# Optimization experiments

Measured on AMD Instinct MI355X. Metric: run time of the kernel, lower is better.

Reference implementation:

```python
import math
import jax, jax.numpy as jnp
import numpy as np

X_DIM = 512
Y_DIM = 512
DS = 4
WH, WW = Y_DIM // DS, X_DIM // DS
RADIUS = 6          # search_radius
PATCH = 21          # patch_size
SIGMA = 1.0         # preprocess_sigma
DELTA = 0.2
MASK_TH = 0.05
RAIN_TH = 0.1


def _blur(x, sigma=SIGMA):
    # replicate-pad + depthwise 2D gaussian conv (matches _gaussian_blur2d)
    r = max(1, int(math.ceil(3.0 * sigma)))
    c = jnp.arange(-r, r + 1, dtype=x.dtype)
    k1 = jnp.exp(-(c * c) / (2.0 * sigma * sigma))
    k1 = k1 / jnp.sum(k1)
    k2 = jnp.outer(k1, k1)
    C = x.shape[1]
    kern = jnp.broadcast_to(k2[None, None], (C, 1, 2 * r + 1, 2 * r + 1))
    xp = jnp.pad(x, ((0, 0), (0, 0), (r, r), (r, r)), mode='edge')
    return jax.lax.conv_general_dilated(xp, kern, (1, 1), 'VALID',
                                        dimension_numbers=('NCHW', 'OIHW', 'NCHW'),
                                        feature_group_count=C)


def _resize(x, oh, ow):
    # torch bilinear, align_corners=False, no antialias
    ih, iw = x.shape[-2], x.shape[-1]
    def coords(o, i):
        s = (jnp.arange(o, dtype=jnp.float32) + 0.5) * (i / o) - 0.5
        s = jnp.maximum(s, 0.0)
        i0 = jnp.minimum(jnp.floor(s).astype(jnp.int32), i - 1)
        i1 = jnp.minimum(i0 + 1, i - 1)
        return i0, i1, s - i0.astype(jnp.float32)
    y0, y1, wy = coords(oh, ih)
    x0, x1, wx = coords(ow, iw)
    r0 = x[..., y0, :]
    r1 = x[..., y1, :]
    v00 = r0[..., x0]; v01 = r0[..., x1]
    v10 = r1[..., x0]; v11 = r1[..., x1]
    wy = wy[:, None]; wx = wx[None, :]
    return v00 * (1 - wy) * (1 - wx) + v01 * (1 - wy) * wx + v10 * wy * (1 - wx) + v11 * wy * wx


def _avg_pool(x, k):
    # avg_pool2d, stride 1, padding k//2, count_include_pad=True
    p = k // 2
    nd = x.ndim
    win = (1,) * (nd - 2) + (k, k)
    pads = ((0, 0),) * (nd - 2) + ((p, p), (p, p))
    s = jax.lax.reduce_window(x, 0.0, jax.lax.add, win, (1,) * nd, pads)
    return s / float(k * k)


def _prepare(f):
    w = jnp.log1p(jnp.maximum(f, 0.0))
    w = _resize(w, WH, WW)
    return _blur(w)


def _grid_sample_border(field, grid):
    # bilinear grid_sample, padding_mode='border', align_corners=True
    B, C, H, W = field.shape
    ix = jnp.clip((grid[..., 0] + 1.0) * 0.5 * (W - 1), 0.0, W - 1)
    iy = jnp.clip((grid[..., 1] + 1.0) * 0.5 * (H - 1), 0.0, H - 1)
    x0 = jnp.floor(ix).astype(jnp.int32); y0 = jnp.floor(iy).astype(jnp.int32)
    x1 = jnp.minimum(x0 + 1, W - 1); y1 = jnp.minimum(y0 + 1, H - 1)
    wx = (ix - x0)[..., None]; wy = (iy - y0)[..., None]
    b = jnp.arange(B)[:, None, None]
    v00 = field[b, :, y0, x0]; v01 = field[b, :, y0, x1]
    v10 = field[b, :, y1, x0]; v11 = field[b, :, y1, x1]  # each [B,H,W,C]
    out = v00 * (1 - wy) * (1 - wx) + v01 * (1 - wy) * wx + v10 * wy * (1 - wx) + v11 * wy * wx
    return jnp.transpose(out, (0, 3, 1, 2))


def setup_inputs() -> dict:
    key = jax.random.key(0)
    k1, k2, k3 = jax.random.split(key, 3)
    pred = jax.random.normal(k1, (16, 1, 512, 512), dtype=jnp.float32)
    target = jax.random.uniform(k2, (16, 1, 512, 512), dtype=jnp.float32)
    ref = jax.random.uniform(k3, (16, 1, 512, 512), dtype=jnp.float32)
    return {"pred": pred, "target": target, "ref": ref}


def reference(pred, target, ref):
    prev_w = _prepare(ref)      # [B,1,WH,WW]
    curr_w = _prepare(target)
    rain = (_resize(target, WH, WW) >= RAIN_TH).astype(jnp.float32)
    n = 2 * RADIUS + 1
    offs = jnp.arange(-RADIUS, RADIUS + 1)
    dys = jnp.repeat(offs, n)   # dy outer loop
    dxs = jnp.tile(offs, n)     # dx inner loop
    rows = jnp.arange(WH); cols = jnp.arange(WW)

    def shift_cost(dy, dx):
        # replicate-border shift of curr_w by (dy,dx), then local SSD (21x21 avg)
        sh = curr_w[:, :, jnp.clip(rows + dy, 0, WH - 1), :]
        sh = sh[:, :, :, jnp.clip(cols + dx, 0, WW - 1)]
        return _avg_pool((prev_w - sh) ** 2, PATCH)

    costs = jax.vmap(shift_cost)(dys, dxs)        # [S,B,1,WH,WW]
    best = jnp.argmin(costs, axis=0)[:, 0]        # [B,WH,WW] (first-min, matches torch)
    fx = dxs.astype(jnp.float32)[best][:, None] * rain   # [B,1,WH,WW]
    fy = dys.astype(jnp.float32)[best][:, None] * rain
    fx = _blur(fx) * rain
    fy = _blur(fy) * rain
    fx = _resize(fx, Y_DIM, X_DIM) * (X_DIM / WW)
    fy = _resize(fy, Y_DIM, X_DIM) * (Y_DIM / WH)

    yy, xx = jnp.meshgrid(jnp.linspace(-1.0, 1.0, Y_DIM),
                          jnp.linspace(-1.0, 1.0, X_DIM), indexing='ij')
    gx = xx[None] - fx[:, 0] * (2.0 / (X_DIM - 1))
    gy = yy[None] - fy[:, 0] * (2.0 / (Y_DIM - 1))
    teacher = jnp.maximum(_grid_sample_border(ref, jnp.stack([gx, gy], axis=-1)), 0.0)

    d = pred - teacher
    ad = jnp.abs(d)
    loss = jnp.where(ad < DELTA, 0.5 * d * d, DELTA * (ad - 0.5 * DELTA))  # huber
    mask = ((teacher > MASK_TH) | (target > MASK_TH)).astype(loss.dtype)
    return jnp.mean(loss * mask)
```

## Files before the change

kernel.cpp:

```cpp
#include <hip/hip_runtime.h>
#include <math.h>

#define BATCH 16
#define HR 512
#define LR 128
#define N_LR (BATCH*LR*LR)
#define N_HR (BATCH*HR*HR)
#define NSH 13
#define NSHIFT 169
#define TH 8
#define CW 16

__device__ __forceinline__ int clampi(int v, int lo, int hi){ return v<lo?lo:(v>hi?hi:v); }

__device__ __forceinline__ float gk(int t){
  const float e1 = 0.60653065971263342f;
  const float e2 = 0.13533528323661270f;
  const float e3 = 0.011108996538242306f;
  const float norm = 1.0f/(1.0f + 2.0f*(e1+e2+e3));
  int a = t < 0 ? -t : t;
  float v = (a==0) ? 1.0f : (a==1 ? e1 : (a==2 ? e2 : e3));
  return v*norm;
}

__global__ void k_downsample(const float* __restrict__ ref, const float* __restrict__ tar,
                             float* __restrict__ wref, float* __restrict__ wtar,
                             float* __restrict__ rain){
  int i = blockIdx.x*blockDim.x + threadIdx.x;
  if (i >= N_LR) return;
  int x = i & (LR-1); int y = (i >> 7) & (LR-1); int b = i >> 14;
  int base = b*HR*HR + (4*y+1)*HR + 4*x;
  float4 r1 = *(const float4*)(ref + base);
  float4 r2 = *(const float4*)(ref + base + HR);
  float4 t1 = *(const float4*)(tar + base);
  float4 t2 = *(const float4*)(tar + base + HR);
  float r00=r1.y, r01=r1.z, r10=r2.y, r11=r2.z;
  float t00=t1.y, t01=t1.z, t10=t2.y, t11=t2.z;
  wref[i] = 0.25f*(log1pf(fmaxf(r00,0.f))+log1pf(fmaxf(r01,0.f))
                 +log1pf(fmaxf(r10,0.f))+log1pf(fmaxf(r11,0.f)));
  wtar[i] = 0.25f*(log1pf(fmaxf(t00,0.f))+log1pf(fmaxf(t01,0.f))
                 +log1pf(fmaxf(t10,0.f))+log1pf(fmaxf(t11,0.f)));
  rain[i] = (0.25f*(t00+t01+t10+t11) >= 0.1f) ? 1.0f : 0.0f;
}

__global__ void k_blur2(const float* __restrict__ in0, const float* __restrict__ in1,
                        float* __restrict__ out0, float* __restrict__ out1,
                        const float* __restrict__ m0, const float* __restrict__ m1){
  const int z = blockIdx.z;
  const float* in  = z ? in1 : in0;
  float* out       = z ? out1 : out0;
  const float* msk = z ? m1 : m0;
  const int r0 = blockIdx.x * 16;
  const int bb = blockIdx.y;
  const int tid = threadIdx.x;
  const float* I = in + (bb<<14);
  __shared__ float raw[22][LR];
  __shared__ float hb[22][LR];
  for (int idx = tid; idx < 22*LR; idx += 256){
    int lr = idx >> 7, c = idx & (LR-1);
    int gr = clampi(r0 - 3 + lr, 0, LR-1);
    raw[lr][c] = I[(gr<<7) + c];
  }
  __syncthreads();
  for (int idx = tid; idx < 22*LR; idx += 256){
    int lr = idx >> 7, c = idx & (LR-1);
    float s = 0.f;
    #pragma unroll
    for (int t=-3;t<=3;++t) s += gk(t)*raw[lr][clampi(c+t,0,LR-1)];
    hb[lr][c] = s;
  }
  __syncthreads();
  for (int idx = tid; idx < 16*LR; idx += 256){
    int lr = idx >> 7, c = idx & (LR-1);
    int i = r0 + lr;
    float s = 0.f;
    #pragma unroll
    for (int t=-3;t<=3;++t) s += gk(t)*hb[clampi(i+t,0,LR-1) - (r0-3)][c];
    int gi = (bb<<14) + (i<<7) + c;
    if (msk) s *= msk[gi];
    out[gi] = s;
  }
}

__global__ void __launch_bounds__(1024)
k_cost_flow(const float* __restrict__ prev, const float* __restrict__ curr,
            const float* __restrict__ rain,
            float* __restrict__ fx, float* __restrict__ fy){
  const int r0 = blockIdx.x * TH;
  const int bb = blockIdx.y;
  const int tid = threadIdx.x;
  const int w = tid >> 6, lane = tid & 63;
  const int j0 = 2*lane;
  const float* P = prev + (bb<<14);
  const float* C = curr + (bb<<14);

  __shared__ __align__(16) union {
    struct { float prevT[28][LR]; float currT[40][140]; } t;
    unsigned long long merge[4][TH*LR];
  } sh;
  __shared__ float pfx[CW][LR];

  for (int idx = tid; idx < 28*LR; idx += 1024){
    int lr = idx >> 7, c = idx & (LR-1);
    int gr = r0 - 10 + lr;
    if (gr >= 0 && gr < LR) sh.t.prevT[lr][c] = P[(gr<<7) + c];
  }
  for (int idx = tid; idx < 40*140; idx += 1024){
    int lr = idx / 140, c = idx - lr*140;
    int gr = r0 - 16 + lr;
    if (gr >= 0 && gr < LR) sh.t.currT[lr][c] = C[(gr<<7) + clampi(c-6,0,LR-1)];
  }
  __syncthreads();

  unsigned long long bk0[TH], bk1[TH];
  #pragma unroll
  for (int io=0; io<TH; ++io){ bk0[io] = ~0ULL; bk1[io] = ~0ULL; }

  for (int s = w; s < NSHIFT; s += CW){
    const int dy = s/NSH - 6, dx = s%NSH - 6;
    const int cb = dx + 6;
    float V0[TH], V1[TH];
    float v0 = 0.f, v1 = 0.f;
    #pragma unroll
    for (int u = -10; u <= 10; ++u){
      int r = r0 + u;
      if (r < 0 || r >= LR) continue;
      int lr = u + 10;
      int cr = clampi(r + dy, 0, LR-1) - r0 + 16;
      float2 p = *(const float2*)&sh.t.prevT[lr][j0];
      float c0 = sh.t.currT[cr][j0 + cb];
      float c1 = sh.t.currT[cr][j0 + 1 + cb];
      float d0 = p.x - c0, d1 = p.y - c1;
      v0 = fmaf(d0,d0,v0); v1 = fmaf(d1,d1,v1);
    }
    V0[0] = v0; V1[0] = v1;
    #pragma unroll
    for (int io = 1; io < TH; ++io){
      int i = r0 + io;
      int ra = i + 10;
      if (ra < LR){
        int lr = ra - r0 + 10;
        int cr = clampi(ra + dy, 0, LR-1) - r0 + 16;
        float2 p = *(const float2*)&sh.t.prevT[lr][j0];
        float c0 = sh.t.currT[cr][j0 + cb];
        float c1 = sh.t.currT[cr][j0 + 1 + cb];
        float d0 = p.x - c0, d1 = p.y - c1;
        v0 = fmaf(d0,d0,v0); v1 = fmaf(d1,d1,v1);
      }
      int rs = i - 11;
      if (rs >= 0){
        int lr = rs - r0 + 10;
        int cr = clampi(rs + dy, 0, LR-1) - r0 + 16;
        float2 p = *(const float2*)&sh.t.prevT[lr][j0];
        float c0 = sh.t.currT[cr][j0 + cb];
        float c1 = sh.t.currT[cr][j0 + 1 + cb];
        float d0 = p.x - c0, d1 = p.y - c1;
        v0 -= d0*d0; v1 -= d1*d1;
      }
      V0[io] = v0; V1[io] = v1;
    }
    #pragma unroll
    for (int io = 0; io < TH; ++io){
      float t = V0[io] + V1[io];
      float x = t;
      #pragma unroll
      for (int d = 1; d < 64; d <<= 1){
        float y = __shfl_up(x, d, 64);
        if (lane >= d) x += y;
      }
      float excl = x - t;
      float p0 = excl + V0[io];
      float p1 = p0 + V1[io];
      *(float2*)&pfx[w][j0] = make_float2(p0, p1);
      float a0 = pfx[w][min(j0+10, LR-1)];
      float a1 = pfx[w][min(j0+11, LR-1)];
      float b0r = pfx[w][max(j0-11, 0)];
      float b1r = pfx[w][max(j0-10, 0)];
      float b0 = (j0 >= 11) ? b0r : 0.f;
      float b1 = (j0 >= 10) ? b1r : 0.f;
      float c0 = fmaxf((a0-b0)*(1.0f/441.0f), 0.f);
      float c1 = fmaxf((a1-b1)*(1.0f/441.0f), 0.f);
      unsigned long long k0 = ((unsigned long long)__float_as_uint(c0)<<32) | (unsigned)s;
      unsigned long long k1 = ((unsigned long long)__float_as_uint(c1)<<32) | (unsigned)s;
      if (k0 < bk0[io]) bk0[io] = k0;
      if (k1 < bk1[io]) bk1[io] = k1;
    }
  }

  __syncthreads();
  const int g = w & 3;
  #pragma unroll
  for (int round = 0; round < 4; ++round){
    if ((w >> 2) == round){
      if (round == 0){
        #pragma unroll
        for (int io = 0; io < TH; ++io){
          sh.merge[g][io*LR + j0]     = bk0[io];
          sh.merge[g][io*LR + j0 + 1] = bk1[io];
        }
      } else {
        #pragma unroll
        for (int io = 0; io < TH; ++io){
          unsigned long long m0 = sh.merge[g][io*LR + j0];
          unsigned long long m1 = sh.merge[g][io*LR + j0 + 1];
          sh.merge[g][io*LR + j0]     = (bk0[io] < m0) ? bk0[io] : m0;
          sh.merge[g][io*LR + j0 + 1] = (bk1[io] < m1) ? bk1[io] : m1;
        }
      }
    }
    __syncthreads();
  }
  {
    int p = tid;
    unsigned long long k = sh.merge[0][p];
    unsigned long long k1 = sh.merge[1][p]; if (k1 < k) k = k1;
    unsigned long long k2 = sh.merge[2][p]; if (k2 < k) k = k2;
    unsigned long long k3 = sh.merge[3][p]; if (k3 < k) k = k3;
    int s = (int)(k & 0xffffffffULL);
    int io = p >> 7, jj = p & (LR-1);
    int gi = (bb<<14) + ((r0+io)<<7) + jj;
    float r = rain[gi];
    fx[gi] = (float)(s % NSH - 6) * r;
    fy[gi] = (float)(s / NSH - 6) * r;
  }
}

__global__ void __launch_bounds__(256)
k_loss(const float* __restrict__ pred, const float* __restrict__ tar,
       const float* __restrict__ ref, const float* __restrict__ fxb,
       const float* __restrict__ fyb, float* __restrict__ out){
  const int nthreads = gridDim.x * 256;
  float acc = 0.f;
  for (int gq = blockIdx.x*256 + threadIdx.x; gq < N_HR/4; gq += nthreads){
    int b   = gq >> 16;
    int rem = gq & 65535;
    int y   = rem >> 7;
    int x4  = (rem & 127) << 2;
    float sy = fmaxf(0.25f*(float)y - 0.375f, 0.f);
    int y0 = min((int)sy, LR-1); int y1 = min(y0+1, LR-1); float wy = sy - (float)y0;
    int lb = b<<14;
    const float* Fx0 = fxb + lb + (y0<<7);
    const float* Fx1 = fxb + lb + (y1<<7);
    const float* Fy0 = fyb + lb + (y0<<7);
    const float* Fy1 = fyb + lb + (y1<<7);
    int hb = (b<<18) + (y<<9) + x4;
    float4 pd = *(const float4*)(pred + hb);
    float4 td = *(const float4*)(tar + hb);
    const float* R = ref + (b<<18);
    #pragma unroll
    for (int k = 0; k < 4; ++k){
      int x = x4 + k;
      float sx = fmaxf(0.25f*(float)x - 0.375f, 0.f);
      int x0 = min((int)sx, LR-1); int x1 = min(x0+1, LR-1); float wx = sx - (float)x0;
      float w00=(1.f-wy)*(1.f-wx), w01=(1.f-wy)*wx, w10=wy*(1.f-wx), w11=wy*wx;
      float fxv = 4.f*(w00*Fx0[x0] + w01*Fx0[x1] + w10*Fx1[x0] + w11*Fx1[x1]);
      float fyv = 4.f*(w00*Fy0[x0] + w01*Fy0[x1] + w10*Fy1[x0] + w11*Fy1[x1]);
      float ix = fminf(fmaxf((float)x - fxv, 0.f), (float)(HR-1));
      float iy = fminf(fmaxf((float)y - fyv, 0.f), (float)(HR-1));
      int gx0 = (int)ix; int gx1 = min(gx0+1, HR-1); float gwx = ix - (float)gx0;
      int gy0 = (int)iy; int gy1 = min(gy0+1, HR-1); float gwy = iy - (float)gy0;
      float v00 = R[(gy0<<9)+gx0], v01 = R[(gy0<<9)+gx1];
      float v10 = R[(gy1<<9)+gx0], v11 = R[(gy1<<9)+gx1];
      float t = v00*(1.f-gwy)*(1.f-gwx) + v01*(1.f-gwy)*gwx
              + v10*gwy*(1.f-gwx)       + v11*gwy*gwx;
      float teacher = fmaxf(t, 0.f);
      float pk = ((const float*)&pd)[k];
      float tk = ((const float*)&td)[k];
      float d  = pk - teacher;
      float ad = fabsf(d);
      float l  = ad < 0.2f ? 0.5f*d*d : 0.2f*(ad - 0.1f);
      float m  = (teacher > 0.05f || tk > 0.05f) ? 1.f : 0.f;
      acc += l*m;
    }
  }
  acc *= (1.0f/(float)N_HR);
  #pragma unroll
  for (int o = 32; o > 0; o >>= 1) acc += __shfl_down(acc, o, 64);
  __shared__ float wsum[4];
  int lane = threadIdx.x & 63, wv = threadIdx.x >> 6;
  if (lane == 0) wsum[wv] = acc;
  __syncthreads();
  if (threadIdx.x == 0) atomicAdd(out, wsum[0]+wsum[1]+wsum[2]+wsum[3]);
}

extern "C" void kernel_launch(void* const* d_in, const int* in_sizes, int n_in,
                              void* d_out, int out_size, void* d_ws, size_t ws_size,
                              hipStream_t stream){
  const float* pred = (const float*)d_in[0];
  const float* tar  = (const float*)d_in[1];
  const float* ref  = (const float*)d_in[2];
  float* out = (float*)d_out;
  float* w = (float*)d_ws;
  float* prevW = w + 0*N_LR;
  float* currW = w + 1*N_LR;
  float* rain  = w + 2*N_LR;
  float* fxb   = w + 3*N_LR;
  float* fyb   = w + 4*N_LR;
  float* dsA   = w + 5*N_LR;
  float* dsB   = w + 6*N_LR;

  hipMemsetAsync(d_out, 0, sizeof(float), stream);

  const int tb = 256, nb = (N_LR + tb - 1)/tb;
  k_downsample<<<nb, tb, 0, stream>>>(ref, tar, dsA, dsB, rain);
  k_blur2<<<dim3(8, BATCH, 2), tb, 0, stream>>>(dsA, dsB, prevW, currW, nullptr, nullptr);
  k_cost_flow<<<dim3(LR/TH, BATCH), 1024, 0, stream>>>(prevW, currW, rain, dsA, dsB);
  k_blur2<<<dim3(8, BATCH, 2), tb, 0, stream>>>(dsA, dsB, fxb, fyb, rain, rain);
  k_loss<<<2048, tb, 0, stream>>>(pred, tar, ref, fxb, fyb, out);
}
```

Baseline: 217.2 us.

## Restructure cost-flow with register-resident rows, DPP prefix scans, and simplified loss upsampling

New measurement: 191.2 us. -11.9%, faster.

```diff
diff --git a/kernel.cpp b/kernel.cpp
--- a/kernel.cpp
+++ b/kernel.cpp
@@ -9,7 +9,7 @@
 #define NSH 13
 #define NSHIFT 169
 #define TH 8
-#define CW 16
+#define NW 8
 
 __device__ __forceinline__ int clampi(int v, int lo, int hi){ return v<lo?lo:(v>hi?hi:v); }
 
@@ -82,7 +82,45 @@
   }
 }
 
-__global__ void __launch_bounds__(1024)
+template<int CTRL, int RM>
+__device__ __forceinline__ float dpp_mov0(float x){
+  return __int_as_float(__builtin_amdgcn_update_dpp(0, __float_as_int(x), CTRL, RM, 0xF, true));
+}
+__device__ __forceinline__ float prefix64(float x){
+  x += dpp_mov0<0x111,0xF>(x);
+  x += dpp_mov0<0x112,0xF>(x);
+  x += dpp_mov0<0x114,0xF>(x);
+  x += dpp_mov0<0x118,0xF>(x);
+  x += dpp_mov0<0x142,0xA>(x);
+  x += dpp_mov0<0x143,0xC>(x);
+  return x;
+}
+__device__ __forceinline__ float bperm(int addr4, float v){
+  return __int_as_float(__builtin_amdgcn_ds_bpermute(addr4, __float_as_int(v)));
+}
+
+struct TapCtx { int ia0, ib0, ia1, ib1; bool la0hi, lb0ok, lb1hi, selA, selB; };
+
+__device__ __forceinline__ void horiz_update(const TapCtx& tc, float v0, float v1, int s,
+                                             unsigned long long& k0ref, unsigned long long& k1ref){
+  float pf0 = prefix64(v0);
+  float pf1 = prefix64(v1);
+  float T0 = __int_as_float(__builtin_amdgcn_readlane(__float_as_int(pf0), 63));
+  float va = tc.selA ? pf0 : pf1;
+  float vb = tc.selB ? pf0 : pf1;
+  float a0 = bperm(tc.ia0, va) + (tc.la0hi ? T0 : 0.f);
+  float b0 = tc.lb0ok ? bperm(tc.ib0, pf0) : 0.f;
+  float a1 = bperm(tc.ia1, pf1) + T0;
+  float b1 = bperm(tc.ib1, vb) + (tc.lb1hi ? T0 : 0.f);
+  float c0 = fmaxf((a0 - b0) * (1.0f/441.0f), 0.f);
+  float c1 = fmaxf((a1 - b1) * (1.0f/441.0f), 0.f);
+  unsigned long long k0 = ((unsigned long long)__float_as_uint(c0) << 32) | (unsigned)s;
+  unsigned long long k1 = ((unsigned long long)__float_as_uint(c1) << 32) | (unsigned)s;
+  if (k0 < k0ref) k0ref = k0;
+  if (k1 < k1ref) k1ref = k1;
+}
+
+__global__ void __launch_bounds__(512, 2)
 k_cost_flow(const float* __restrict__ prev, const float* __restrict__ curr,
             const float* __restrict__ rain,
             float* __restrict__ fx, float* __restrict__ fy){
@@ -90,132 +128,128 @@
   const int bb = blockIdx.y;
   const int tid = threadIdx.x;
   const int w = tid >> 6, lane = tid & 63;
-  const int j0 = 2*lane;
   const float* P = prev + (bb<<14);
   const float* C = curr + (bb<<14);
 
-  __shared__ __align__(16) union {
-    struct { float prevT[28][LR]; float currT[40][140]; } t;
-    unsigned long long merge[4][TH*LR];
-  } sh;
-  __shared__ float pfx[CW][LR];
-
-  for (int idx = tid; idx < 28*LR; idx += 1024){
+  __shared__ float currT[40][LR];
+  __shared__ unsigned long long mg[4][TH*LR];
+
+  for (int idx = tid; idx < 40*LR; idx += 512){
     int lr = idx >> 7, c = idx & (LR-1);
-    int gr = r0 - 10 + lr;
-    if (gr >= 0 && gr < LR) sh.t.prevT[lr][c] = P[(gr<<7) + c];
-  }
-  for (int idx = tid; idx < 40*140; idx += 1024){
-    int lr = idx / 140, c = idx - lr*140;
-    int gr = r0 - 16 + lr;
-    if (gr >= 0 && gr < LR) sh.t.currT[lr][c] = C[(gr<<7) + clampi(c-6,0,LR-1)];
+    int gr = clampi(r0 - 16 + lr, 0, LR-1);
+    currT[lr][c] = C[(gr<<7) + c];
+  }
+
+  float p0[28], p1[28];
+  #pragma unroll
+  for (int wr = 0; wr < 28; ++wr){
+    int gr = r0 - 10 + wr;
+    if (gr >= 0 && gr < LR){ p0[wr] = P[(gr<<7) + lane]; p1[wr] = P[(gr<<7) + lane + 64]; }
+    else                   { p0[wr] = 0.f; p1[wr] = 0.f; }
   }
   __syncthreads();
 
   unsigned long long bk0[TH], bk1[TH];
   #pragma unroll
-  for (int io=0; io<TH; ++io){ bk0[io] = ~0ULL; bk1[io] = ~0ULL; }
-
-  for (int s = w; s < NSHIFT; s += CW){
-    const int dy = s/NSH - 6, dx = s%NSH - 6;
-    const int cb = dx + 6;
-    float V0[TH], V1[TH];
-    float v0 = 0.f, v1 = 0.f;
-    #pragma unroll
-    for (int u = -10; u <= 10; ++u){
-      int r = r0 + u;
-      if (r < 0 || r >= LR) continue;
-      int lr = u + 10;
-      int cr = clampi(r + dy, 0, LR-1) - r0 + 16;
-      float2 p = *(const float2*)&sh.t.prevT[lr][j0];
-      float c0 = sh.t.currT[cr][j0 + cb];
-      float c1 = sh.t.currT[cr][j0 + 1 + cb];
-      float d0 = p.x - c0, d1 = p.y - c1;
-      v0 = fmaf(d0,d0,v0); v1 = fmaf(d1,d1,v1);
-    }
-    V0[0] = v0; V1[0] = v1;
-    #pragma unroll
-    for (int io = 1; io < TH; ++io){
-      int i = r0 + io;
-      int ra = i + 10;
-      if (ra < LR){
-        int lr = ra - r0 + 10;
-        int cr = clampi(ra + dy, 0, LR-1) - r0 + 16;
-        float2 p = *(const float2*)&sh.t.prevT[lr][j0];
-        float c0 = sh.t.currT[cr][j0 + cb];
-        float c1 = sh.t.currT[cr][j0 + 1 + cb];
-        float d0 = p.x - c0, d1 = p.y - c1;
-        v0 = fmaf(d0,d0,v0); v1 = fmaf(d1,d1,v1);
-      }
-      int rs = i - 11;
-      if (rs >= 0){
-        int lr = rs - r0 + 10;
-        int cr = clampi(rs + dy, 0, LR-1) - r0 + 16;
-        float2 p = *(const float2*)&sh.t.prevT[lr][j0];
-        float c0 = sh.t.currT[cr][j0 + cb];
-        float c1 = sh.t.currT[cr][j0 + 1 + cb];
-        float d0 = p.x - c0, d1 = p.y - c1;
-        v0 -= d0*d0; v1 -= d1*d1;
-      }
-      V0[io] = v0; V1[io] = v1;
-    }
-    #pragma unroll
-    for (int io = 0; io < TH; ++io){
-      float t = V0[io] + V1[io];
-      float x = t;
+  for (int io = 0; io < TH; ++io){ bk0[io] = ~0ULL; bk1[io] = ~0ULL; }
+
+  TapCtx tc;
+  tc.ia0 = ((lane + 10) & 63) << 2;
+  tc.ib0 = ((lane - 11) & 63) << 2;
+  tc.ia1 = (min(lane + 10, 63)) << 2;
+  tc.ib1 = ((lane + 53) & 63) << 2;
+  tc.la0hi = (lane >= 54);
+  tc.lb0ok = (lane >= 11);
+  tc.lb1hi = (lane >= 11);
+  tc.selA  = (lane >= 10);
+  tc.selB  = (lane >= 53);
+
+  const int t_lo = (NSHIFT * w) / NW;
+  const int t_hi = (NSHIFT * (w+1)) / NW;
+
+  int t = t_lo;
+  while (t < t_hi){
+    const int dxi  = t / NSH;
+    const int dyi0 = t - dxi*NSH;
+    const int ndy  = min(NSH - dyi0, t_hi - t);
+    const int dx   = dxi - 6;
+    const int c0   = clampi(lane + dx, 0, LR-1);
+    const int c1   = clampi(lane + 64 + dx, 0, LR-1);
+    float q0[28], q1[28];
+    #pragma unroll
+    for (int wr = 0; wr < 28; ++wr){
+      q0[wr] = currT[wr + dyi0][c0];
+      q1[wr] = currT[wr + dyi0][c1];
+    }
+    int s = dyi0*NSH + dxi;
+    for (int rep = 0; rep < ndy; ++rep){
+      float v0 = 0.f, v1 = 0.f;
       #pragma unroll
-      for (int d = 1; d < 64; d <<= 1){
-        float y = __shfl_up(x, d, 64);
-        if (lane >= d) x += y;
-      }
-      float excl = x - t;
-      float p0 = excl + V0[io];
-      float p1 = p0 + V1[io];
-      *(float2*)&pfx[w][j0] = make_float2(p0, p1);
-      float a0 = pfx[w][min(j0+10, LR-1)];
-      float a1 = pfx[w][min(j0+11, LR-1)];
-      float b0r = pfx[w][max(j0-11, 0)];
-      float b1r = pfx[w][max(j0-10, 0)];
-      float b0 = (j0 >= 11) ? b0r : 0.f;
-      float b1 = (j0 >= 10) ? b1r : 0.f;
-      float c0 = fmaxf((a0-b0)*(1.0f/441.0f), 0.f);
-      float c1 = fmaxf((a1-b1)*(1.0f/441.0f), 0.f);
-      unsigned long long k0 = ((unsigned long long)__float_as_uint(c0)<<32) | (unsigned)s;
-      unsigned long long k1 = ((unsigned long long)__float_as_uint(c1)<<32) | (unsigned)s;
-      if (k0 < bk0[io]) bk0[io] = k0;
-      if (k1 < bk1[io]) bk1[io] = k1;
-    }
-  }
-
-  __syncthreads();
-  const int g = w & 3;
-  #pragma unroll
-  for (int round = 0; round < 4; ++round){
-    if ((w >> 2) == round){
-      if (round == 0){
-        #pragma unroll
-        for (int io = 0; io < TH; ++io){
-          sh.merge[g][io*LR + j0]     = bk0[io];
-          sh.merge[g][io*LR + j0 + 1] = bk1[io];
-        }
-      } else {
-        #pragma unroll
-        for (int io = 0; io < TH; ++io){
-          unsigned long long m0 = sh.merge[g][io*LR + j0];
-          unsigned long long m1 = sh.merge[g][io*LR + j0 + 1];
-          sh.merge[g][io*LR + j0]     = (bk0[io] < m0) ? bk0[io] : m0;
-          sh.merge[g][io*LR + j0 + 1] = (bk1[io] < m1) ? bk1[io] : m1;
+      for (int wr = 0; wr <= 20; ++wr){
+        if (r0 - 10 + wr >= 0 && r0 - 10 + wr < LR){
+          float d0 = p0[wr] - q0[wr];
+          float d1 = p1[wr] - q1[wr];
+          v0 = fmaf(d0, d0, v0);
+          v1 = fmaf(d1, d1, v1);
         }
       }
-    }
-    __syncthreads();
-  }
-  {
-    int p = tid;
-    unsigned long long k = sh.merge[0][p];
-    unsigned long long k1 = sh.merge[1][p]; if (k1 < k) k = k1;
-    unsigned long long k2 = sh.merge[2][p]; if (k2 < k) k = k2;
-    unsigned long long k3 = sh.merge[3][p]; if (k3 < k) k = k3;
+      horiz_update(tc, v0, v1, s, bk0[0], bk1[0]);
+      #pragma unroll
+      for (int io = 1; io < TH; ++io){
+        {
+          const int wrA = io + 20;
+          if (r0 - 10 + wrA < LR){
+            float d0 = p0[wrA] - q0[wrA];
+            float d1 = p1[wrA] - q1[wrA];
+            v0 = fmaf(d0, d0, v0);
+            v1 = fmaf(d1, d1, v1);
+          }
+          const int wrS = io - 1;
+          if (r0 - 10 + wrS >= 0){
+            float d0 = p0[wrS] - q0[wrS];
+            float d1 = p1[wrS] - q1[wrS];
+            v0 = fmaf(-d0, d0, v0);
+            v1 = fmaf(-d1, d1, v1);
+          }
+        }
+        horiz_update(tc, v0, v1, s, bk0[io], bk1[io]);
+      }
+      if (rep < ndy - 1){
+        #pragma unroll
+        for (int wr = 0; wr < 27; ++wr){ q0[wr] = q0[wr+1]; q1[wr] = q1[wr+1]; }
+        q0[27] = currT[dyi0 + rep + 28][c0];
+        q1[27] = currT[dyi0 + rep + 28][c1];
+      }
+      s += NSH;
+    }
+    t += ndy;
+  }
+
+  __syncthreads();
+  const int g = w & 3;
+  if (w < 4){
+    #pragma unroll
+    for (int io = 0; io < TH; ++io){
+      mg[g][io*LR + lane]      = bk0[io];
+      mg[g][io*LR + lane + 64] = bk1[io];
+    }
+  }
+  __syncthreads();
+  if (w >= 4){
+    #pragma unroll
+    for (int io = 0; io < TH; ++io){
+      unsigned long long m0 = mg[g][io*LR + lane];
+      unsigned long long m1 = mg[g][io*LR + lane + 64];
+      mg[g][io*LR + lane]      = (bk0[io] < m0) ? bk0[io] : m0;
+      mg[g][io*LR + lane + 64] = (bk1[io] < m1) ? bk1[io] : m1;
+    }
+  }
+  __syncthreads();
+  for (int p = tid; p < TH*LR; p += 512){
+    unsigned long long k  = mg[0][p];
+    unsigned long long k1 = mg[1][p]; if (k1 < k) k = k1;
+    unsigned long long k2 = mg[2][p]; if (k2 < k) k = k2;
+    unsigned long long k3 = mg[3][p]; if (k3 < k) k = k3;
     int s = (int)(k & 0xffffffffULL);
     int io = p >> 7, jj = p & (LR-1);
     int gi = (bb<<14) + ((r0+io)<<7) + jj;
@@ -229,48 +263,71 @@
 k_loss(const float* __restrict__ pred, const float* __restrict__ tar,
        const float* __restrict__ ref, const float* __restrict__ fxb,
        const float* __restrict__ fyb, float* __restrict__ out){
-  const int nthreads = gridDim.x * 256;
+  const int t0 = blockIdx.x*256 + threadIdx.x;
   float acc = 0.f;
-  for (int gq = blockIdx.x*256 + threadIdx.x; gq < N_HR/4; gq += nthreads){
-    int b   = gq >> 16;
-    int rem = gq & 65535;
-    int y   = rem >> 7;
-    int x4  = (rem & 127) << 2;
-    float sy = fmaxf(0.25f*(float)y - 0.375f, 0.f);
-    int y0 = min((int)sy, LR-1); int y1 = min(y0+1, LR-1); float wy = sy - (float)y0;
-    int lb = b<<14;
-    const float* Fx0 = fxb + lb + (y0<<7);
-    const float* Fx1 = fxb + lb + (y1<<7);
-    const float* Fy0 = fyb + lb + (y0<<7);
-    const float* Fy1 = fyb + lb + (y1<<7);
-    int hb = (b<<18) + (y<<9) + x4;
+  #pragma unroll
+  for (int it = 0; it < 2; ++it){
+    const int gq  = t0 + it*524288;
+    const int b   = gq >> 16;
+    const int rem = gq & 65535;
+    const int y   = rem >> 7;
+    const int m   = rem & 127;
+    const int n = y >> 2, ky = y & 3;
+    int y0; float wy;
+    if (ky < 2){ y0 = max(n-1, 0); wy = (n >= 1) ? (ky == 0 ? 0.625f : 0.875f) : 0.f; }
+    else       { y0 = n;           wy = (ky == 2) ? 0.125f : 0.375f; }
+    const int y1 = min(y0+1, LR-1);
+    const int lb = b << 14;
+    const float* FxR0 = fxb + lb + (y0<<7);
+    const float* FxR1 = fxb + lb + (y1<<7);
+    const float* FyR0 = fyb + lb + (y0<<7);
+    const float* FyR1 = fyb + lb + (y1<<7);
+    const int cA = max(m-1, 0), cB = m, cC = min(m+1, LR-1);
+    float xA0 = FxR0[cA], xB0 = FxR0[cB], xC0 = FxR0[cC];
+    float xA1 = FxR1[cA], xB1 = FxR1[cB], xC1 = FxR1[cC];
+    float yA0 = FyR0[cA], yB0 = FyR0[cB], yC0 = FyR0[cC];
+    float yA1 = FyR1[cA], yB1 = FyR1[cB], yC1 = FyR1[cC];
+    const bool mh = (m >= 1);
+    const int hb = (b<<18) + (y<<9) + (m<<2);
     float4 pd = *(const float4*)(pred + hb);
     float4 td = *(const float4*)(tar + hb);
     const float* R = ref + (b<<18);
+    const float wy1 = 1.f - wy;
     #pragma unroll
     for (int k = 0; k < 4; ++k){
-      int x = x4 + k;
-      float sx = fmaxf(0.25f*(float)x - 0.375f, 0.f);
-      int x0 = min((int)sx, LR-1); int x1 = min(x0+1, LR-1); float wx = sx - (float)x0;
-      float w00=(1.f-wy)*(1.f-wx), w01=(1.f-wy)*wx, w10=wy*(1.f-wx), w11=wy*wx;
-      float fxv = 4.f*(w00*Fx0[x0] + w01*Fx0[x1] + w10*Fx1[x0] + w11*Fx1[x1]);
-      float fyv = 4.f*(w00*Fy0[x0] + w01*Fy0[x1] + w10*Fy1[x0] + w11*Fy1[x1]);
+      float wx;
+      float lo0, hi0, lo1, hi1, flo0, fhi0, flo1, fhi1;
+      if (k < 2){
+        wx = mh ? (k == 0 ? 0.625f : 0.875f) : 0.f;
+        lo0 = mh ? xA0 : xB0;  hi0 = mh ? xB0 : xC0;
+        lo1 = mh ? xA1 : xB1;  hi1 = mh ? xB1 : xC1;
+        flo0 = mh ? yA0 : yB0; fhi0 = mh ? yB0 : yC0;
+        flo1 = mh ? yA1 : yB1; fhi1 = mh ? yB1 : yC1;
+      } else {
+        wx = (k == 2) ? 0.125f : 0.375f;
+        lo0 = xB0;  hi0 = xC0;  lo1 = xB1;  hi1 = xC1;
+        flo0 = yB0; fhi0 = yC0; flo1 = yB1; fhi1 = yC1;
+      }
+      const float w00 = wy1*(1.f-wx), w01 = wy1*wx, w10 = wy*(1.f-wx), w11 = wy*wx;
+      const float fxv = 4.f*(w00*lo0 + w01*hi0 + w10*lo1 + w11*hi1);
+      const float fyv = 4.f*(w00*flo0 + w01*fhi0 + w10*flo1 + w11*fhi1);
+      const int x = (m<<2) + k;
       float ix = fminf(fmaxf((float)x - fxv, 0.f), (float)(HR-1));
       float iy = fminf(fmaxf((float)y - fyv, 0.f), (float)(HR-1));
       int gx0 = (int)ix; int gx1 = min(gx0+1, HR-1); float gwx = ix - (float)gx0;
       int gy0 = (int)iy; int gy1 = min(gy0+1, HR-1); float gwy = iy - (float)gy0;
       float v00 = R[(gy0<<9)+gx0], v01 = R[(gy0<<9)+gx1];
       float v10 = R[(gy1<<9)+gx0], v11 = R[(gy1<<9)+gx1];
-      float t = v00*(1.f-gwy)*(1.f-gwx) + v01*(1.f-gwy)*gwx
-              + v10*gwy*(1.f-gwx)       + v11*gwy*gwx;
-      float teacher = fmaxf(t, 0.f);
+      float tt = v00*(1.f-gwy)*(1.f-gwx) + v01*(1.f-gwy)*gwx
+               + v10*gwy*(1.f-gwx)       + v11*gwy*gwx;
+      float teacher = fmaxf(tt, 0.f);
       float pk = ((const float*)&pd)[k];
       float tk = ((const float*)&td)[k];
       float d  = pk - teacher;
       float ad = fabsf(d);
       float l  = ad < 0.2f ? 0.5f*d*d : 0.2f*(ad - 0.1f);
-      float m  = (teacher > 0.05f || tk > 0.05f) ? 1.f : 0.f;
-      acc += l*m;
+      float mm = (teacher > 0.05f || tk > 0.05f) ? 1.f : 0.f;
+      acc += l*mm;
     }
   }
   acc *= (1.0f/(float)N_HR);
@@ -304,7 +361,7 @@
   const int tb = 256, nb = (N_LR + tb - 1)/tb;
   k_downsample<<<nb, tb, 0, stream>>>(ref, tar, dsA, dsB, rain);
   k_blur2<<<dim3(8, BATCH, 2), tb, 0, stream>>>(dsA, dsB, prevW, currW, nullptr, nullptr);
-  k_cost_flow<<<dim3(LR/TH, BATCH), 1024, 0, stream>>>(prevW, currW, rain, dsA, dsB);
+  k_cost_flow<<<dim3(LR/TH, BATCH), 512, 0, stream>>>(prevW, currW, rain, dsA, dsB);
   k_blur2<<<dim3(8, BATCH, 2), tb, 0, stream>>>(dsA, dsB, fxb, fyb, rain, rain);
   k_loss<<<2048, tb, 0, stream>>>(pred, tar, ref, fxb, fyb, out);
 }
```
